# Kernel optimization log

Measured on AMD Instinct MI355X. Metric: run time of the kernel, lower is better.

## Reference

```python
import jax, jax.numpy as jnp
import numpy as np

NUM_ENTS = 100000
NUM_RELS = 237
IN_CH, OUT_CH, KER = 1, 32, 9
IN_DIM = 200
K = 10
OUT_DIM = K * IN_DIM                      # 2000
L_IN = OUT_DIM // IN_CH                   # 2000
L_OUT = (L_IN - KER) // 1 + 1             # 1992
FC_LEN = OUT_CH * L_OUT                   # 63744
BATCH = 512
EPS = 1e-5


def _bn(x, gamma, beta, axes):
    # training-mode batch norm (biased variance), matching torch BatchNorm1d forward
    m = jnp.mean(x, axis=axes, keepdims=True)
    v = jnp.var(x, axis=axes, keepdims=True)
    return (x - m) * jax.lax.rsqrt(v + EPS) * gamma + beta


def setup_inputs() -> dict:
    key = jax.random.key(0)
    ks = jax.random.split(key, 8)
    xavier = lambda k, shape, fan: jax.random.normal(k, shape, jnp.float32) * np.sqrt(2.0 / fan)
    E = xavier(ks[0], (NUM_ENTS, IN_DIM), NUM_ENTS + IN_DIM)
    R = xavier(ks[1], (NUM_RELS * 2, OUT_CH, IN_CH, KER), OUT_CH * IN_CH * KER)
    e_W = xavier(ks[2], (IN_DIM, OUT_DIM), IN_DIM + OUT_DIM)
    fc_W = xavier(ks[3], (IN_DIM, FC_LEN), IN_DIM + FC_LEN)  # torch Linear weight [out, in]
    return {
        "E": E, "R": R, "e_W": e_W, "fc_W": fc_W,
        "bn0_gamma": jnp.ones((IN_DIM,), jnp.float32), "bn0_beta": jnp.zeros((IN_DIM,), jnp.float32),
        "bn1_gamma": jnp.ones((OUT_CH,), jnp.float32), "bn1_beta": jnp.zeros((OUT_CH,), jnp.float32),
        "bn2_gamma": jnp.ones((IN_DIM,), jnp.float32), "bn2_beta": jnp.zeros((IN_DIM,), jnp.float32),
        "e1_idx": jax.random.randint(ks[4], (BATCH,), 0, NUM_ENTS),
        "r_idx": jax.random.randint(ks[5], (BATCH,), 0, NUM_RELS * 2),
    }


def reference(E, R, e_W, fc_W, bn0_gamma, bn0_beta, bn1_gamma, bn1_beta,
              bn2_gamma, bn2_beta, e1_idx, r_idx):
    B = e1_idx.shape[0]
    x = E[e1_idx]                                   # [B, 200]
    x = _bn(x, bn0_gamma, bn0_beta, axes=0)
    x = x @ e_W                                     # [B, 2000]
    k = R[r_idx]                                    # [B, O, C, KER] per-sample filters
    x = x.reshape(B, IN_CH, L_IN)                   # [B, C, L_in]
    # per-sample grouped conv1d == batched small matmul over sliding windows
    win = jnp.arange(L_OUT)[:, None] + jnp.arange(KER)[None, :]  # [L_out, KER]
    patches = x[:, :, win]                          # [B, C, L_out, KER]
    x = jnp.einsum('bock,bclk->bol', k, patches)    # [B, O, L_out]
    x = _bn(x, bn1_gamma[:, None], bn1_beta[:, None], axes=(0, 2))
    x = x.reshape(B, FC_LEN)
    x = x @ fc_W.T                                  # [B, 200]
    x = jnp.tanh(_bn(x, bn2_gamma, bn2_beta, axes=0))
    logits = x @ E.T                                # [B, num_ents]
    return jax.nn.sigmoid(logits)
```

## Files before the change

### kernel.cpp

```cpp
#include <hip/hip_runtime.h>

#define NENT 100000
#define DIM 200
#define ODIM 2000
#define KERN 9
#define OCH 32
#define LOUT 1992
#define FCLEN 63744
#define BSZ 512
#define EPSV 1e-5f
#define KPAD 224
#define NZ 64
#define EROWS 100096

typedef float f32x4 __attribute__((ext_vector_type(4)));
typedef short short8 __attribute__((ext_vector_type(8)));
typedef __bf16 bf16x8 __attribute__((ext_vector_type(8)));
typedef unsigned int uint4v __attribute__((ext_vector_type(4)));
typedef unsigned int uint2v __attribute__((ext_vector_type(2)));

__device__ __forceinline__ unsigned short f2bf(float f) {
  unsigned int u = __float_as_uint(f);
  return (unsigned short)((u + 0x7fffu + ((u >> 16) & 1u)) >> 16);
}

__device__ __forceinline__ float wredf(float v) {
#pragma unroll
  for (int o = 32; o > 0; o >>= 1) v += __shfl_down(v, o, 64);
  return v;
}

__global__ void k_init(float* bias) {
  int t = threadIdx.x;
  if (t < DIM) bias[t] = 0.f;
}

__global__ void __launch_bounds__(256) k_ebf(const float* __restrict__ E,
                                             unsigned short* __restrict__ Ebf) {
  long idx = (long)blockIdx.x * 256 + threadIdx.x;
  int row = (int)(idx / 56), c4 = (int)(idx % 56);
  f32x4 v = (f32x4){0.f, 0.f, 0.f, 0.f};
  if (row < NENT && c4 < 50) v = *(const f32x4*)&E[(long)row * DIM + c4 * 4];
  uint2v pk;
  pk[0] = (unsigned)f2bf(v[0]) | ((unsigned)f2bf(v[1]) << 16);
  pk[1] = (unsigned)f2bf(v[2]) | ((unsigned)f2bf(v[3]) << 16);
  *(uint2v*)&Ebf[(long)row * KPAD + c4 * 4] = pk;
}

__global__ void k_bn0(const float* __restrict__ E, const int* __restrict__ e1,
                      const float* __restrict__ g, const float* __restrict__ b,
                      float* __restrict__ A, float* __restrict__ Bc) {
  int f = blockIdx.x, ln = threadIdx.x;
  float s1 = 0.f, s2 = 0.f;
  for (int i = ln; i < BSZ; i += 64) {
    float v = E[(long)e1[i] * DIM + f];
    s1 += v; s2 += v * v;
  }
  s1 = wredf(s1); s2 = wredf(s2);
  if (ln == 0) {
    float m = s1 / BSZ;
    float var = s2 / BSZ - m * m;
    float a = g[f] * rsqrtf(var + EPSV);
    A[f] = a; Bc[f] = b[f] - m * a;
  }
}

__global__ void __launch_bounds__(256) k_mm1(
    const float* __restrict__ E, const int* __restrict__ e1,
    const float* __restrict__ eW, const float* __restrict__ A,
    const float* __restrict__ Bc, float* __restrict__ x1) {
  __shared__ float xs[16][DIM];
  int t = threadIdx.x;
  int b0 = blockIdx.x * 16, n0 = blockIdx.y * 128;
  for (int idx = t; idx < 16 * DIM; idx += 256) {
    int bi = idx / DIM, f = idx % DIM;
    xs[bi][f] = E[(long)e1[b0 + bi] * DIM + f] * A[f] + Bc[f];
  }
  __syncthreads();
  int lane = t & 63, w = t >> 6;
  int j0 = n0 + lane, j1 = j0 + 64;
  int r0 = w * 4;
  bool c0 = (j0 < ODIM), c1 = (j1 < ODIM);
  float acc[4][2];
#pragma unroll
  for (int r = 0; r < 4; r++) { acc[r][0] = 0.f; acc[r][1] = 0.f; }
  for (int k = 0; k < DIM; k += 4) {
    f32x4 xr[4];
#pragma unroll
    for (int r = 0; r < 4; r++) xr[r] = *(const f32x4*)&xs[r0 + r][k];
#pragma unroll
    for (int kk = 0; kk < 4; kk++) {
      float e0v = c0 ? eW[(long)(k + kk) * ODIM + j0] : 0.f;
      float e1v = c1 ? eW[(long)(k + kk) * ODIM + j1] : 0.f;
#pragma unroll
      for (int r = 0; r < 4; r++) {
        acc[r][0] += xr[r][kk] * e0v;
        acc[r][1] += xr[r][kk] * e1v;
      }
    }
  }
#pragma unroll
  for (int r = 0; r < 4; r++) {
    long base = (long)(b0 + r0 + r) * ODIM;
    if (c0) x1[base + j0] = acc[r][0];
    if (c1) x1[base + j1] = acc[r][1];
  }
}

__global__ void __launch_bounds__(256) k_conv(
    const float* __restrict__ x1, const float* __restrict__ R,
    const int* __restrict__ ridx, unsigned short* __restrict__ convb,
    float* __restrict__ part) {
  __shared__ float xs[ODIM];
  __shared__ float kr[OCH * KERN];
  __shared__ float wr4[4][64];
  int t = threadIdx.x, b = blockIdx.x;
  for (int i = t; i < ODIM; i += 256) xs[i] = x1[(long)b * ODIM + i];
  for (int i = t; i < OCH * KERN; i += 256) kr[i] = R[(long)ridx[b] * (OCH * KERN) + i];
  __syncthreads();
  int l0 = t * 8;
  bool act = (t < 249);
  float w[16];
  if (act) {
#pragma unroll
    for (int i = 0; i < 16; i++) w[i] = xs[l0 + i];
  }
  int wv = t >> 6, ln = t & 63;
  for (int o = 0; o < OCH; o++) {
    float s1 = 0.f, s2 = 0.f;
    if (act) {
      float kk[KERN];
#pragma unroll
      for (int k = 0; k < KERN; k++) kk[k] = kr[o * KERN + k];
      float cb[8];
#pragma unroll
      for (int j = 0; j < 8; j++) {
        float c = 0.f;
#pragma unroll
        for (int k = 0; k < KERN; k++) c += kk[k] * w[j + k];
        cb[j] = c; s1 += c; s2 += c * c;
      }
      uint4v pk;
#pragma unroll
      for (int i = 0; i < 4; i++)
        pk[i] = (unsigned)f2bf(cb[2 * i]) | ((unsigned)f2bf(cb[2 * i + 1]) << 16);
      *(uint4v*)(convb + (long)b * FCLEN + o * LOUT + l0) = pk;
    }
    s1 = wredf(s1); s2 = wredf(s2);
    if (ln == 0) { wr4[wv][o] = s1; wr4[wv][o + 32] = s2; }
  }
  __syncthreads();
  if (t < 64) part[(long)b * 64 + t] = wr4[0][t] + wr4[1][t] + wr4[2][t] + wr4[3][t];
}

__global__ void k_bn1fin(const float* __restrict__ part, const float* __restrict__ g,
                         const float* __restrict__ b, float* __restrict__ a,
                         float* __restrict__ c) {
  __shared__ float sm[4][64];
  __shared__ float tot[64];
  int t = threadIdx.x;
  int si = t >> 6, st = t & 63;
  float s = 0.f;
  for (int i = si; i < BSZ; i += 4) s += part[(long)i * 64 + st];
  sm[si][st] = s;
  __syncthreads();
  if (t < 64) tot[t] = sm[0][t] + sm[1][t] + sm[2][t] + sm[3][t];
  __syncthreads();
  if (t < OCH) {
    float N = (float)BSZ * LOUT;
    float m = tot[t] / N;
    float var = tot[t + 32] / N - m * m;
    float av = g[t] * rsqrtf(var + EPSV);
    a[t] = av; c[t] = b[t] - m * av;
  }
}

__global__ void __launch_bounds__(256) k_fcw(
    const float* __restrict__ fcW, const float* __restrict__ a,
    const float* __restrict__ c, unsigned short* __restrict__ fcWb,
    float* __restrict__ bias) {
  int d = blockIdx.x, o = blockIdx.y, t = threadIdx.x;
  const float* src = fcW + (long)d * FCLEN + o * LOUT;
  unsigned short* dst = fcWb + (long)d * FCLEN + o * LOUT;
  float ao = a[o];
  float s = 0.f;
  if (t < 249) {
    float v[8];
#pragma unroll
    for (int j = 0; j < 8; j++) { v[j] = src[t * 8 + j]; s += v[j]; }
    uint4v pk;
#pragma unroll
    for (int i = 0; i < 4; i++)
      pk[i] = (unsigned)f2bf(v[2 * i] * ao) | ((unsigned)f2bf(v[2 * i + 1] * ao) << 16);
    *(uint4v*)(dst + t * 8) = pk;
  }
  s = wredf(s);
  __shared__ float sm[4];
  if ((t & 63) == 0) sm[t >> 6] = s;
  __syncthreads();
  if (t == 0) atomicAdd(bias + d, c[o] * (sm[0] + sm[1] + sm[2] + sm[3]));
}

__global__ void __launch_bounds__(256) k_gemm_fc(
    const unsigned short* __restrict__ convb, const unsigned short* __restrict__ fcWb,
    float* __restrict__ ypart) {
  __shared__ unsigned short lA[128 * 104];
  __shared__ unsigned short lB[128 * 104];
  int t = threadIdx.x;
  int b0 = blockIdx.x * 128, n0 = blockIdx.y * 128, z = blockIdx.z;
  int s0 = (664 * z) / NZ, s1 = (664 * (z + 1)) / NZ;
  int w = t >> 6, lane = t & 63, lm = lane & 15, quad = lane >> 4;
  int mq = (w >> 1) * 64, nq = (w & 1) * 64;
  f32x4 acc[4][4];
#pragma unroll
  for (int mi = 0; mi < 4; mi++)
#pragma unroll
    for (int ni = 0; ni < 4; ni++) acc[mi][ni] = (f32x4){0.f, 0.f, 0.f, 0.f};
  for (int st = s0; st < s1; st++) {
    long kc = (long)st * 96;
    __syncthreads();
#pragma unroll
    for (int i = 0; i < 6; i++) {
      int cc = t + 256 * i;
      int row = cc / 12, c8 = cc % 12;
      *(uint4v*)&lA[row * 104 + c8 * 8] =
          *(const uint4v*)&convb[(long)(b0 + row) * FCLEN + kc + c8 * 8];
      uint4v bv = (uint4v){0u, 0u, 0u, 0u};
      int nr = n0 + row;
      if (nr < DIM) bv = *(const uint4v*)&fcWb[(long)nr * FCLEN + kc + c8 * 8];
      *(uint4v*)&lB[row * 104 + c8 * 8] = bv;
    }
    __syncthreads();
#pragma unroll
    for (int ks = 0; ks < 96; ks += 32) {
      short8 af[4], bfr[4];
#pragma unroll
      for (int i2 = 0; i2 < 4; i2++) {
        af[i2] = *(const short8*)&lA[(mq + i2 * 16 + lm) * 104 + ks + quad * 8];
        bfr[i2] = *(const short8*)&lB[(nq + i2 * 16 + lm) * 104 + ks + quad * 8];
      }
#pragma unroll
      for (int mi = 0; mi < 4; mi++)
#pragma unroll
        for (int ni = 0; ni < 4; ni++)
          acc[mi][ni] = __builtin_amdgcn_mfma_f32_16x16x32_bf16(
              __builtin_bit_cast(bf16x8, af[mi]), __builtin_bit_cast(bf16x8, bfr[ni]),
              acc[mi][ni], 0, 0, 0);
    }
  }
#pragma unroll
  for (int mi = 0; mi < 4; mi++)
#pragma unroll
    for (int ni = 0; ni < 4; ni++)
#pragma unroll
      for (int r = 0; r < 4; r++) {
        int gm = b0 + mq + mi * 16 + quad * 4 + r;
        int gn = n0 + nq + ni * 16 + lm;
        ypart[((long)z * BSZ + gm) * 256 + gn] = acc[mi][ni][r];
      }
}

__global__ void __launch_bounds__(256) k_yred(
    const float* __restrict__ ypart, const float* __restrict__ bias,
    float* __restrict__ y) {
  int i = blockIdx.x * 256 + threadIdx.x;
  int m = i / DIM, d = i % DIM;
  float s = bias[d];
#pragma unroll 8
  for (int z = 0; z < NZ; z++) s += ypart[((long)z * BSZ + m) * 256 + d];
  y[(long)m * DIM + d] = s;
}

__global__ void k_bn2(const float* __restrict__ y, const float* __restrict__ g,
                      const float* __restrict__ b, unsigned short* __restrict__ xt) {
  int d = blockIdx.x, ln = threadIdx.x;
  if (d >= DIM) {
    for (int i = ln; i < BSZ; i += 64) xt[(long)i * KPAD + d] = 0;
    return;
  }
  float v[8];
  float s1 = 0.f, s2 = 0.f;
#pragma unroll
  for (int j = 0; j < 8; j++) {
    v[j] = y[(long)(ln + 64 * j) * DIM + d];
    s1 += v[j]; s2 += v[j] * v[j];
  }
  s1 = wredf(s1); s2 = wredf(s2);
  s1 = __shfl(s1, 0, 64); s2 = __shfl(s2, 0, 64);
  float m = s1 / BSZ, var = s2 / BSZ - m * m;
  float a = g[d] * rsqrtf(var + EPSV), c = b[d] - m * a;
#pragma unroll
  for (int j = 0; j < 8; j++)
    xt[(long)(ln + 64 * j) * KPAD + d] = f2bf(tanhf(v[j] * a + c));
}

__global__ void __launch_bounds__(256, 4) k_gemmf(
    const unsigned short* __restrict__ xt, const unsigned short* __restrict__ Ebf,
    float* __restrict__ out) {
  int t = threadIdx.x;
  int w = t >> 6, lane = t & 63, lm = lane & 15, quad = lane >> 4;
  long ew = (long)blockIdx.x * 256 + w * 64;
  int m0 = blockIdx.y * 64;
  f32x4 acc[4][4];
#pragma unroll
  for (int mi = 0; mi < 4; mi++)
#pragma unroll
    for (int ni = 0; ni < 4; ni++) acc[mi][ni] = (f32x4){0.f, 0.f, 0.f, 0.f};
  for (int kk = 0; kk < 7; kk++) {
    int k0 = kk * 32;
    short8 bfr[4], af[4];
#pragma unroll
    for (int ni = 0; ni < 4; ni++)
      bfr[ni] = *(const short8*)&Ebf[(ew + ni * 16 + lm) * KPAD + k0 + quad * 8];
#pragma unroll
    for (int mi = 0; mi < 4; mi++)
      af[mi] = *(const short8*)&xt[(long)(m0 + mi * 16 + lm) * KPAD + k0 + quad * 8];
#pragma unroll
    for (int mi = 0; mi < 4; mi++)
#pragma unroll
      for (int ni = 0; ni < 4; ni++)
        acc[mi][ni] = __builtin_amdgcn_mfma_f32_16x16x32_bf16(
            __builtin_bit_cast(bf16x8, af[mi]), __builtin_bit_cast(bf16x8, bfr[ni]),
            acc[mi][ni], 0, 0, 0);
  }
#pragma unroll
  for (int mi = 0; mi < 4; mi++)
#pragma unroll
    for (int ni = 0; ni < 4; ni++)
#pragma unroll
      for (int r = 0; r < 4; r++) {
        int gb = m0 + mi * 16 + quad * 4 + r;
        long ge = ew + ni * 16 + lm;
        if (ge < NENT) {
          float x = acc[mi][ni][r];
          out[(long)gb * NENT + ge] = 1.f / (1.f + __expf(-x));
        }
      }
}

extern "C" void kernel_launch(void* const* d_in, const int* in_sizes, int n_in,
                              void* d_out, int out_size, void* d_ws, size_t ws_size,
                              hipStream_t stream) {
  const float* E = (const float*)d_in[0];
  const float* R = (const float*)d_in[1];
  const float* eW = (const float*)d_in[2];
  const float* fcW = (const float*)d_in[3];
  const float* bn0g = (const float*)d_in[4];
  const float* bn0b = (const float*)d_in[5];
  const float* bn1g = (const float*)d_in[6];
  const float* bn1b = (const float*)d_in[7];
  const float* bn2g = (const float*)d_in[8];
  const float* bn2b = (const float*)d_in[9];
  const int* e1 = (const int*)d_in[10];
  const int* ridx = (const int*)d_in[11];
  float* outp = (float*)d_out;

  char* p = (char*)d_ws;
  size_t off = 0;
  auto alloc = [&](size_t bytes) -> char* {
    char* r = p + off;
    off = (off + bytes + 255) & ~(size_t)255;
    return r;
  };
  float* x1 = (float*)alloc((size_t)BSZ * ODIM * 4);
  unsigned short* convb = (unsigned short*)alloc((size_t)BSZ * FCLEN * 2);
  unsigned short* fcWb = (unsigned short*)alloc((size_t)DIM * FCLEN * 2);
  unsigned short* Ebf = (unsigned short*)alloc((size_t)EROWS * KPAD * 2);
  float* ypart = (float*)alloc((size_t)NZ * BSZ * 256 * 4);
  float* y = (float*)alloc((size_t)BSZ * DIM * 4);
  unsigned short* xt = (unsigned short*)alloc((size_t)BSZ * KPAD * 2);
  float* bn0A = (float*)alloc(DIM * 4);
  float* bn0B = (float*)alloc(DIM * 4);
  float* part = (float*)alloc((size_t)BSZ * 64 * 4);
  float* bn1a = (float*)alloc(OCH * 4);
  float* bn1c = (float*)alloc(OCH * 4);
  float* bias = (float*)alloc(DIM * 4);

  k_init<<<1, 256, 0, stream>>>(bias);
  k_ebf<<<(EROWS * 56) / 256, 256, 0, stream>>>(E, Ebf);
  k_bn0<<<DIM, 64, 0, stream>>>(E, e1, bn0g, bn0b, bn0A, bn0B);
  k_mm1<<<dim3(32, 16), 256, 0, stream>>>(E, e1, eW, bn0A, bn0B, x1);
  k_conv<<<BSZ, 256, 0, stream>>>(x1, R, ridx, convb, part);
  k_bn1fin<<<1, 256, 0, stream>>>(part, bn1g, bn1b, bn1a, bn1c);
  k_fcw<<<dim3(DIM, OCH), 256, 0, stream>>>(fcW, bn1a, bn1c, fcWb, bias);
  k_gemm_fc<<<dim3(4, 2, NZ), 256, 0, stream>>>(convb, fcWb, ypart);
  k_yred<<<400, 256, 0, stream>>>(ypart, bias, y);
  k_bn2<<<KPAD, 64, 0, stream>>>(y, bn2g, bn2b, xt);
  k_gemmf<<<dim3(391, 8), 256, 0, stream>>>(xt, Ebf, outp);
}
```

Before: 572.0 us.

## Stage final GEMM output through LDS for coalesced vector stores; pre-swizzle A operand

```diff
diff --git a/kernel.cpp b/kernel.cpp
--- a/kernel.cpp
+++ b/kernel.cpp
@@ -272,10 +272,14 @@
 }
 
 __global__ void k_bn2(const float* __restrict__ y, const float* __restrict__ g,
-                      const float* __restrict__ b, unsigned short* __restrict__ xt) {
+                      const float* __restrict__ b, unsigned short* __restrict__ xtf) {
   int d = blockIdx.x, ln = threadIdx.x;
+  int ks = d >> 5, quad = (d >> 3) & 3, e = d & 7;
   if (d >= DIM) {
-    for (int i = ln; i < BSZ; i += 64) xt[(long)i * KPAD + d] = 0;
+    for (int j = 0; j < 8; j++) {
+      int row = ln + 64 * j;
+      xtf[((((long)(row >> 4) * 7 + ks) * 64) + quad * 16 + (row & 15)) * 8 + e] = 0;
+    }
     return;
   }
   float v[8];
@@ -290,17 +294,22 @@
   float m = s1 / BSZ, var = s2 / BSZ - m * m;
   float a = g[d] * rsqrtf(var + EPSV), c = b[d] - m * a;
 #pragma unroll
-  for (int j = 0; j < 8; j++)
-    xt[(long)(ln + 64 * j) * KPAD + d] = f2bf(tanhf(v[j] * a + c));
+  for (int j = 0; j < 8; j++) {
+    int row = ln + 64 * j;
+    xtf[((((long)(row >> 4) * 7 + ks) * 64) + quad * 16 + (row & 15)) * 8 + e] =
+        f2bf(tanhf(v[j] * a + c));
+  }
 }
 
 __global__ void __launch_bounds__(256, 4) k_gemmf(
-    const unsigned short* __restrict__ xt, const unsigned short* __restrict__ Ebf,
+    const unsigned short* __restrict__ xtf, const unsigned short* __restrict__ Ebf,
     float* __restrict__ out) {
+  __shared__ float lds[32][260];
   int t = threadIdx.x;
   int w = t >> 6, lane = t & 63, lm = lane & 15, quad = lane >> 4;
   long ew = (long)blockIdx.x * 256 + w * 64;
   int m0 = blockIdx.y * 64;
+  int mtb = blockIdx.y * 4;
   f32x4 acc[4][4];
 #pragma unroll
   for (int mi = 0; mi < 4; mi++)
@@ -314,7 +323,7 @@
       bfr[ni] = *(const short8*)&Ebf[(ew + ni * 16 + lm) * KPAD + k0 + quad * 8];
 #pragma unroll
     for (int mi = 0; mi < 4; mi++)
-      af[mi] = *(const short8*)&xt[(long)(m0 + mi * 16 + lm) * KPAD + k0 + quad * 8];
+      af[mi] = *(const short8*)&xtf[(((long)(mtb + mi) * 7 + kk) * 64 + lane) * 8];
 #pragma unroll
     for (int mi = 0; mi < 4; mi++)
 #pragma unroll
@@ -323,19 +332,32 @@
             __builtin_bit_cast(bf16x8, af[mi]), __builtin_bit_cast(bf16x8, bfr[ni]),
             acc[mi][ni], 0, 0, 0);
   }
-#pragma unroll
-  for (int mi = 0; mi < 4; mi++)
-#pragma unroll
-    for (int ni = 0; ni < 4; ni++)
-#pragma unroll
-      for (int r = 0; r < 4; r++) {
-        int gb = m0 + mi * 16 + quad * 4 + r;
-        long ge = ew + ni * 16 + lm;
-        if (ge < NENT) {
-          float x = acc[mi][ni][r];
-          out[(long)gb * NENT + ge] = 1.f / (1.f + __expf(-x));
-        }
+  long ge = (long)blockIdx.x * 256 + lane * 4;
+#pragma unroll
+  for (int h = 0; h < 2; h++) {
+    if (h) __syncthreads();
+#pragma unroll
+    for (int mh = 0; mh < 2; mh++) {
+      int mi = 2 * h + mh;
+#pragma unroll
+      for (int ni = 0; ni < 4; ni++)
+#pragma unroll
+        for (int r = 0; r < 4; r++)
+          lds[mh * 16 + quad * 4 + r][w * 64 + ni * 16 + lm] = acc[mi][ni][r];
+    }
+    __syncthreads();
+    if (ge < NENT) {
+#pragma unroll
+      for (int i = 0; i < 8; i++) {
+        int R = w * 8 + i;
+        f32x4 v = *(const f32x4*)&lds[R][lane * 4];
+        f32x4 sg;
+#pragma unroll
+        for (int j = 0; j < 4; j++) sg[j] = 1.f / (1.f + __expf(-v[j]));
+        *(f32x4*)&out[(long)(m0 + 32 * h + R) * NENT + ge] = sg;
       }
+    }
+  }
 }
 
 extern "C" void kernel_launch(void* const* d_in, const int* in_sizes, int n_in,
@@ -368,7 +390,7 @@
   unsigned short* Ebf = (unsigned short*)alloc((size_t)EROWS * KPAD * 2);
   float* ypart = (float*)alloc((size_t)NZ * BSZ * 256 * 4);
   float* y = (float*)alloc((size_t)BSZ * DIM * 4);
-  unsigned short* xt = (unsigned short*)alloc((size_t)BSZ * KPAD * 2);
+  unsigned short* xtf = (unsigned short*)alloc((size_t)BSZ * KPAD * 2);
   float* bn0A = (float*)alloc(DIM * 4);
   float* bn0B = (float*)alloc(DIM * 4);
   float* part = (float*)alloc((size_t)BSZ * 64 * 4);
@@ -385,6 +407,6 @@
   k_fcw<<<dim3(DIM, OCH), 256, 0, stream>>>(fcW, bn1a, bn1c, fcWb, bias);
   k_gemm_fc<<<dim3(4, 2, NZ), 256, 0, stream>>>(convb, fcWb, ypart);
   k_yred<<<400, 256, 0, stream>>>(ypart, bias, y);
-  k_bn2<<<KPAD, 64, 0, stream>>>(y, bn2g, bn2b, xt);
-  k_gemmf<<<dim3(391, 8), 256, 0, stream>>>(xt, Ebf, outp);
-}
+  k_bn2<<<KPAD, 64, 0, stream>>>(y, bn2g, bn2b, xtf);
+  k_gemmf<<<dim3(391, 8), 256, 0, stream>>>(xtf, Ebf, outp);
+}
```

After: 576.5 us. About the same (+0.8%).
